# Performance work log

Measured on AMD Instinct MI355X. Metric: run time of the kernel, lower is better.

The kernel has to match this reference:

```python
import jax, jax.numpy as jnp
import numpy as np

B = 2048
LATENT = 128
C = 8                      # n_classes == class_dim
HID = 1024
D = 512                    # feature dim of minority samples
COUNTS = np.array([1024, 1536, 2048, 2560, 3072, 3584, 3840, 4096])
NMAX = int(COUNTS.max())
NEG = -1e9


def setup_inputs() -> dict:
    key = jax.random.key(0)
    ks = jax.random.split(key, 9)
    z = jax.random.normal(ks[0], (B, LATENT), dtype=jnp.float32)
    class_ids = jax.random.randint(ks[1], (B,), 0, C)
    # cTMU params (stored [in, out]; equivalent to torch Linear with W.T)
    W1 = 0.02 * jax.random.normal(ks[2], (LATENT + C, HID), dtype=jnp.float32)
    b1 = jnp.zeros((HID,), jnp.float32)
    W2 = 0.02 * jax.random.normal(ks[3], (HID, HID), dtype=jnp.float32)
    b2 = jnp.zeros((HID,), jnp.float32)
    # IGU params, padded/stacked over classes: [C, HID, NMAX], [C, NMAX]
    Wa = 0.02 * jax.random.normal(ks[4], (C, HID, NMAX), dtype=jnp.float32)
    ba = jnp.zeros((C, NMAX), jnp.float32)
    # class memory buffers, zero-padded to NMAX: [C, NMAX, D]
    Xbuf = jax.random.normal(ks[5], (C, NMAX, D), dtype=jnp.float32)
    valid = jnp.arange(NMAX)[None, :] < jnp.asarray(COUNTS)[:, None]  # [C, NMAX]
    Xbuf = Xbuf * valid[:, :, None]
    return {"z": z, "class_ids": class_ids, "W1": W1, "b1": b1,
            "W2": W2, "b2": b2, "Wa": Wa, "ba": ba, "Xbuf": Xbuf}


def reference(z, class_ids, W1, b1, W2, b2, Wa, ba, Xbuf):
    # cTMU: concat(z, onehot) -> Linear -> GELU -> Linear -> GELU
    onehot = jax.nn.one_hot(class_ids, C, dtype=z.dtype)       # [B, C]
    x = jnp.concatenate([z, onehot], axis=1)                   # [B, LATENT+C]
    h = jax.nn.gelu(x @ W1 + b1, approximate=False)            # [B, HID]
    t = jax.nn.gelu(h @ W2 + b2, approximate=False)            # [B, HID]
    # IGU logits for every class (grouped GEMM over padded buffers)
    logits = jnp.einsum('bh,chn->bcn', t, Wa) + ba[None]       # [B, C, NMAX]
    valid = jnp.arange(NMAX)[None, :] < jnp.asarray(COUNTS)[:, None]
    logits = jnp.where(valid[None], logits, NEG)
    alpha = jax.nn.softmax(logits, axis=-1)                    # [B, C, NMAX]
    # convex combination against each class buffer, then route by class id
    synth = jnp.einsum('bcn,cnd->bcd', alpha, Xbuf)            # [B, C, D]
    out = synth[jnp.arange(z.shape[0]), class_ids]             # [B, D]
    return out
```

## Files before the change

### kernel.cpp

```cpp
#include <hip/hip_runtime.h>
#include <math.h>


constexpr int B = 2048, LATENT = 128, C = 8, HID = 1024, D = 512, NMAX = 4096;

typedef __attribute__((ext_vector_type(8))) short bf16x8;
typedef __attribute__((ext_vector_type(4))) float f32x4;

#define GLD16(gsrc, ldst)                                                     \
    __builtin_amdgcn_global_load_lds(                                         \
        (const __attribute__((address_space(1))) unsigned int*)(gsrc),        \
        (__attribute__((address_space(3))) unsigned int*)(ldst), 16, 0, 0)

__device__ __forceinline__ int class_count(int c) {
    if (c < 6) return 1024 + 512 * c;
    return (c == 6) ? 3840 : 4096;
}

__device__ __forceinline__ float gelu_exact(float x) {
    return 0.5f * x * (1.0f + erff(x * 0.70710678118654752f));
}

__device__ __forceinline__ unsigned short f2bf(float f) {
    unsigned int u = __float_as_uint(f);
    return (unsigned short)((u + 0x7fffu + ((u >> 16) & 1u)) >> 16);
}

__device__ __forceinline__ float waveMax(float v) {
    #pragma unroll
    for (int o = 32; o > 0; o >>= 1) v = fmaxf(v, __shfl_down(v, o));
    return v;
}
__device__ __forceinline__ float waveSum(float v) {
    #pragma unroll
    for (int o = 32; o > 0; o >>= 1) v += __shfl_down(v, o);
    return v;
}

__global__ void k_gather(const int* __restrict__ cid, int* __restrict__ cnt,
                         int* __restrict__ idx) {
    int b = blockIdx.x * 256 + threadIdx.x;
    if (b < B) {
        int c = cid[b];
        int s = atomicAdd(&cnt[c], 1);
        idx[c * B + s] = b;
    }
}

__global__ void k_f2bf(const float* __restrict__ src,
                       unsigned short* __restrict__ dst, int n4) {
    int i = blockIdx.x * 256 + threadIdx.x;
    if (i < n4) {
        float4 v = *(const float4*)&src[(size_t)i * 4];
        ushort4 o = {f2bf(v.x), f2bf(v.y), f2bf(v.z), f2bf(v.w)};
        *(ushort4*)&dst[(size_t)i * 4] = o;
    }
}

__global__ __launch_bounds__(256) void k_repack_frag(
    const float* __restrict__ src, unsigned short* __restrict__ dst,
    int R, int Cc, size_t srcStride, size_t dstStride, int limitMode) {
    const int cls = blockIdx.z;
    const int rb = blockIdx.x;
    const int c0 = blockIdx.y * 256;
    if (limitMode == 1 && c0 >= class_count(cls)) return;
    if (limitMode == 2 && rb * 32 >= class_count(cls)) return;
    src += (size_t)cls * srcStride;
    dst += (size_t)cls * dstStride;
    __shared__ float T[32][257];
    const int t = threadIdx.x;
    #pragma unroll
    for (int i = 0; i < 8; ++i) {
        int r = i * 4 + (t >> 6);
        int cc = (t & 63) * 4;
        float4 v = *(const float4*)&src[(size_t)(rb * 32 + r) * Cc + c0 + cc];
        T[r][cc] = v.x; T[r][cc + 1] = v.y; T[r][cc + 2] = v.z; T[r][cc + 3] = v.w;
    }
    __syncthreads();
    const int RB = R >> 5;
    #pragma unroll
    for (int i = 0; i < 4; ++i) {
        int ct = i * 4 + (t >> 6);
        int lane = t & 63;
        int n = lane & 15, q = lane >> 4;
        unsigned short tmp[8];
        #pragma unroll
        for (int j = 0; j < 8; ++j) tmp[j] = f2bf(T[q * 8 + j][ct * 16 + n]);
        *(uint4*)&dst[(((size_t)(c0 / 16 + ct)) * RB + rb) * 512 + lane * 8] =
            *(const uint4*)tmp;
    }
}


#define GEMM_PIPE_STAGE(bufsel, APSTEP, BPSTEP)                               \
    do {                                                                      \
        _Pragma("unroll") for (int i = 0; i < 2; ++i)                         \
            GLD16(ap[i] + (APSTEP), AsW + (bufsel) * 4096 + i * 512);         \
        _Pragma("unroll") for (int i = 0; i < 2; ++i)                         \
            GLD16(bp[i] + (BPSTEP), BsW + (bufsel) * 4096 + i * 512);         \
    } while (0)

#define GEMM_PIPE_LOOP(KE, APSTEP, BPSTEP)                                    \
    {                                                                         \
        const int nk_ = (KE) >> 6;                                            \
        {                                                                     \
            const int k0 = 0;                                                 \
            (void)k0;                                                         \
            GEMM_PIPE_STAGE(0, APSTEP, BPSTEP);                               \
        }                                                                     \
        for (int ks_ = 0; ks_ < nk_; ++ks_) {                                 \
            const int p_ = ks_ & 1;                                           \
            if (ks_ + 1 < nk_) {                                              \
                const int k0 = (ks_ + 1) << 6;                                \
                GEMM_PIPE_STAGE(1 - p_, APSTEP, BPSTEP);                      \
                asm volatile("s_waitcnt vmcnt(4)" ::: "memory");              \
            } else {                                                          \
                asm volatile("s_waitcnt vmcnt(0)" ::: "memory");              \
            }                                                                 \
            asm volatile("s_barrier" ::: "memory");                           \
            __builtin_amdgcn_s_setprio(1);                                    \
            _Pragma("unroll") for (int kb = 0; kb < 2; ++kb) {                \
                bf16x8 bfr[4];                                                \
                _Pragma("unroll") for (int f = 0; f < 4; ++f)                 \
                    bfr[f] = *(const bf16x8*)&Bs[p_ * 4096 +                  \
                        (kb * 4 + f) * 512 + lane * 8];                       \
                bf16x8 af = *(const bf16x8*)&As[p_ * 4096 +                   \
                    (wave * 16 + ln) * 64 +                                   \
                    (((kb * 4 + lq) ^ (ln & 7)) * 8)];                        \
                _Pragma("unroll") for (int f = 0; f < 4; ++f)                 \
                    acc[f] = __builtin_amdgcn_mfma_f32_16x16x32_bf16(         \
                        af, bfr[f], acc[f], 0, 0, 0);                         \
            }                                                                 \
            __builtin_amdgcn_s_setprio(0);                                    \
            asm volatile("s_barrier" ::: "memory");                           \
        }                                                                     \
    }

__global__ __launch_bounds__(256, 8) void k_mlp_mfma(
    const unsigned short* __restrict__ A, const unsigned short* __restrict__ Bf,
    const float* __restrict__ bias, const float* __restrict__ Woh,
    const int* __restrict__ cid, unsigned short* __restrict__ Out, int K) {
    const int row0 = blockIdx.x * 64, col0 = blockIdx.y * 64;
    const int KBtot = K >> 5;
    const int t = threadIdx.x, wave = t >> 6, lane = t & 63;
    const int ln = lane & 15, lq = lane >> 4;
    __shared__ __align__(16) unsigned short As[2 * 64 * 64];
    __shared__ __align__(16) unsigned short Bs[2 * 8 * 512];
    const int arowl = lane >> 3;
    const int achk = (lane & 7) ^ arowl;
    const unsigned short* ap[2];
    #pragma unroll
    for (int i = 0; i < 2; ++i)
        ap[i] = A + (size_t)(row0 + wave * 16 + i * 8 + arowl) * K + achk * 8;
    const int kbw = wave >> 1;
    const unsigned short* bp[2];
    #pragma unroll
    for (int i = 0; i < 2; ++i) {
        int f = (wave * 2 + i) & 3;
        bp[i] = Bf + ((size_t)((col0 >> 4) + f) * KBtot + kbw) * 512 + lane * 8;
    }
    unsigned short* AsW = &As[wave * 1024];
    unsigned short* BsW = &Bs[(wave * 2) * 512];
    f32x4 acc[4] = {};
    GEMM_PIPE_LOOP(K, k0, (size_t)(k0 >> 5) * 512)
    #pragma unroll
    for (int reg = 0; reg < 4; ++reg) {
        int r = row0 + wave * 16 + lq * 4 + reg;
        const float* woh = Woh ? &Woh[(size_t)cid[r] * HID] : nullptr;
        #pragma unroll
        for (int f = 0; f < 4; ++f) {
            int col = col0 + f * 16 + ln;
            float v = acc[f][reg] + bias[col];
            if (woh) v += woh[col];
            Out[(size_t)r * HID + col] = f2bf(gelu_exact(v));
        }
    }
}

__global__ __launch_bounds__(256, 8) void k_logits_mfma(
    const unsigned short* __restrict__ T, const unsigned short* __restrict__ Wf,
    const float* __restrict__ ba, const int* __restrict__ cnt,
    const int* __restrict__ idxs, float* __restrict__ L) {
    const int c = blockIdx.y;
    const int count = class_count(c);
    const int n0 = blockIdx.x * 64;
    if (n0 >= count) return;
    const int Mc = cnt[c];
    const int row0 = blockIdx.z * 64;
    if (row0 >= Mc) return;
    const int* idxc = idxs + c * B;
    const unsigned short* Wfc = Wf + (size_t)c * 4194304;
    const int t = threadIdx.x, wave = t >> 6, lane = t & 63;
    const int ln = lane & 15, lq = lane >> 4;
    __shared__ __align__(16) unsigned short As[2 * 64 * 64];
    __shared__ __align__(16) unsigned short Bs[2 * 8 * 512];
    const int arowl = lane >> 3;
    const int achk = (lane & 7) ^ arowl;
    const unsigned short* ap[2];
    #pragma unroll
    for (int i = 0; i < 2; ++i) {
        int g = idxc[min(row0 + wave * 16 + i * 8 + arowl, Mc - 1)];
        ap[i] = T + (size_t)g * HID + achk * 8;
    }
    const int kbw = wave >> 1;
    const unsigned short* bp[2];
    #pragma unroll
    for (int i = 0; i < 2; ++i) {
        int f = (wave * 2 + i) & 3;
        bp[i] = Wfc + ((size_t)((n0 >> 4) + f) * 32 + kbw) * 512 + lane * 8;
    }
    unsigned short* AsW = &As[wave * 1024];
    unsigned short* BsW = &Bs[(wave * 2) * 512];
    f32x4 acc[4] = {};
    GEMM_PIPE_LOOP(HID, k0, (size_t)(k0 >> 5) * 512)
    #pragma unroll
    for (int reg = 0; reg < 4; ++reg) {
        int r = row0 + wave * 16 + lq * 4 + reg;
        if (r < Mc) {
            int g = idxc[r];
            #pragma unroll
            for (int f = 0; f < 4; ++f) {
                int col = n0 + f * 16 + ln;
                L[(size_t)g * NMAX + col] = acc[f][reg] + ba[c * NMAX + col];
            }
        }
    }
}

__global__ __launch_bounds__(256) void k_softmax(const float* __restrict__ L,
                                                 unsigned short* __restrict__ Aout,
                                                 const int* __restrict__ cid) {
    const int b = blockIdx.x;
    const int n = class_count(cid[b]);
    const float* row = L + (size_t)b * NMAX;
    unsigned short* orow = Aout + (size_t)b * NMAX;
    const int t = threadIdx.x;
    float v[16];
    int nv = 0;
    float mx = -INFINITY;
    for (int i = t; i < n; i += 256) {
        float x = row[i];
        v[nv++] = x;
        mx = fmaxf(mx, x);
    }
    __shared__ float red[4], red2[4];
    float wm = waveMax(mx);
    int wid = t >> 6, lid = t & 63;
    if (lid == 0) red[wid] = wm;
    __syncthreads();
    float bmax = fmaxf(fmaxf(red[0], red[1]), fmaxf(red[2], red[3]));
    float s = 0.f;
    #pragma unroll
    for (int j = 0; j < 16; ++j)
        if (j < nv) { v[j] = expf(v[j] - bmax); s += v[j]; }
    float ws_ = waveSum(s);
    if (lid == 0) red2[wid] = ws_;
    __syncthreads();
    float inv = 1.0f / (red2[0] + red2[1] + red2[2] + red2[3]);
    int j = 0;
    for (int i = t; i < n; i += 256) orow[i] = f2bf(v[j++] * inv);
}

__global__ __launch_bounds__(256, 8) void k_synth_mfma(
    const unsigned short* __restrict__ Al, const unsigned short* __restrict__ Xf,
    const int* __restrict__ cnt, const int* __restrict__ idxs,
    float* __restrict__ Out) {
    const int c = blockIdx.y;
    const int count = class_count(c);
    const int dtile = blockIdx.x & 7, kci = blockIdx.x >> 3;
    const int kc0 = kci * 1024;
    if (kc0 >= count) return;
    const int KE = min(kc0 + 1024, count) - kc0;
    const int Mc = cnt[c];
    const int row0 = blockIdx.z * 64;
    if (row0 >= Mc) return;
    const int* idxc = idxs + c * B;
    const unsigned short* Xfc = Xf + (size_t)c * 2097152;
    const int d0 = dtile * 64;
    const int t = threadIdx.x, wave = t >> 6, lane = t & 63;
    const int ln = lane & 15, lq = lane >> 4;
    __shared__ __align__(16) unsigned short As[2 * 64 * 64];
    __shared__ __align__(16) unsigned short Bs[2 * 8 * 512];
    const int arowl = lane >> 3;
    const int achk = (lane & 7) ^ arowl;
    const unsigned short* ap[2];
    #pragma unroll
    for (int i = 0; i < 2; ++i) {
        int g = idxc[min(row0 + wave * 16 + i * 8 + arowl, Mc - 1)];
        ap[i] = Al + (size_t)g * NMAX + kc0 + achk * 8;
    }
    const int kbw = wave >> 1;
    const unsigned short* bp[2];
    #pragma unroll
    for (int i = 0; i < 2; ++i) {
        int f = (wave * 2 + i) & 3;
        bp[i] = Xfc + ((size_t)((d0 >> 4) + f) * 128 + (kc0 >> 5) + kbw) * 512 + lane * 8;
    }
    unsigned short* AsW = &As[wave * 1024];
    unsigned short* BsW = &Bs[(wave * 2) * 512];
    f32x4 acc[4] = {};
    GEMM_PIPE_LOOP(KE, k0, (size_t)(k0 >> 5) * 512)
    #pragma unroll
    for (int reg = 0; reg < 4; ++reg) {
        int r = row0 + wave * 16 + lq * 4 + reg;
        if (r < Mc) {
            int g = idxc[r];
            #pragma unroll
            for (int f = 0; f < 4; ++f)
                atomicAdd(&Out[(size_t)g * D + d0 + f * 16 + ln], acc[f][reg]);
        }
    }
}

extern "C" void kernel_launch(void* const* d_in, const int* in_sizes, int n_in,
                              void* d_out, int out_size, void* d_ws,
                              size_t ws_size, hipStream_t stream) {
    const float* z    = (const float*)d_in[0];
    const int*   cid  = (const int*)d_in[1];
    const float* W1   = (const float*)d_in[2];
    const float* b1   = (const float*)d_in[3];
    const float* W2   = (const float*)d_in[4];
    const float* b2   = (const float*)d_in[5];
    const float* Wa   = (const float*)d_in[6];
    const float* ba   = (const float*)d_in[7];
    const float* Xbuf = (const float*)d_in[8];
    float* out = (float*)d_out;

    char* ws = (char*)d_ws;
    int*            cnt   = (int*)ws;
    int*            idx   = (int*)(ws + 256);
    unsigned short* zbf   = (unsigned short*)(ws + 65792);
    unsigned short* h     = (unsigned short*)(ws + 590080);
    unsigned short* tbuf  = (unsigned short*)(ws + 4784384);
    float*          L     = (float*)(ws + 8978688);
    unsigned short* abuf  = (unsigned short*)(ws + 42533120);
    unsigned short* Wf    = (unsigned short*)(ws + 59310336);
    unsigned short* Xf    = (unsigned short*)(ws + 126419200);
    unsigned short* W2f   = (unsigned short*)(ws + 159973632);
    unsigned short* W1f   = (unsigned short*)(ws + 162070784);

    hipMemsetAsync(cnt, 0, 256, stream);
    k_gather<<<dim3(B / 256), 256, 0, stream>>>(cid, cnt, idx);
    k_f2bf<<<dim3(256), 256, 0, stream>>>(z, zbf, B * LATENT / 4);
    k_repack_frag<<<dim3(4, 4, 1), 256, 0, stream>>>(W1, W1f, 128, HID, 0, 0, 0);
    k_repack_frag<<<dim3(32, 4, 1), 256, 0, stream>>>(W2, W2f, HID, HID, 0, 0, 0);
    k_repack_frag<<<dim3(32, 16, C), 256, 0, stream>>>(
        Wa, Wf, HID, NMAX, (size_t)HID * NMAX, 4194304, 1);
    k_repack_frag<<<dim3(128, 2, C), 256, 0, stream>>>(
        Xbuf, Xf, NMAX, D, (size_t)NMAX * D, 2097152, 2);
    k_mlp_mfma<<<dim3(B / 64, HID / 64), 256, 0, stream>>>(
        zbf, W1f, b1, W1 + (size_t)LATENT * HID, cid, h, LATENT);
    k_mlp_mfma<<<dim3(B / 64, HID / 64), 256, 0, stream>>>(
        h, W2f, b2, nullptr, cid, tbuf, HID);
    k_logits_mfma<<<dim3(NMAX / 64, C, B / 64), 256, 0, stream>>>(
        tbuf, Wf, ba, cnt, idx, L);
    k_softmax<<<dim3(B), 256, 0, stream>>>(L, abuf, cid);
    hipMemsetAsync(out, 0, (size_t)B * D * sizeof(float), stream);
    k_synth_mfma<<<dim3(32, C, B / 64), 256, 0, stream>>>(
        abuf, Xf, cnt, idx, out);
}
```

Baseline: 364.5 us.

## Fuse fp32-to-bf16 conversion of Wa and Xbuf into grouped GEMM B-loads

Drops the two separate repack kernels that converted Wa (128MB fp32) and Xbuf (64MB fp32) into bf16 fragment layout each call. The logits and synth GEMMs now load fp32 B values directly through registers, convert them with v_cvt_pk_bf16 and write them to shared memory during the MFMA phase of the previous stage. This removes a full read-write pass over the large weight buffers. In exchange, the GEMM B loads become strided scalar fp32 loads that each tile re-reads across row blocks, register pressure rises (launch bounds drop to 4 waves), and each tile now converts its B data again.

```diff
diff --git a/kernel.cpp b/kernel.cpp
--- a/kernel.cpp
+++ b/kernel.cpp
@@ -24,6 +24,12 @@
 __device__ __forceinline__ unsigned short f2bf(float f) {
     unsigned int u = __float_as_uint(f);
     return (unsigned short)((u + 0x7fffu + ((u >> 16) & 1u)) >> 16);
+}
+
+__device__ __forceinline__ unsigned int cvt_pk_bf16(float lo, float hi) {
+    unsigned int r;
+    asm volatile("v_cvt_pk_bf16_f32 %0, %1, %2" : "=v"(r) : "v"(lo), "v"(hi));
+    return r;
 }
 
 __device__ __forceinline__ float waveMax(float v) {
@@ -91,7 +97,6 @@
     }
 }
 
-
 #define GEMM_PIPE_STAGE(bufsel, APSTEP, BPSTEP)                               \
     do {                                                                      \
         _Pragma("unroll") for (int i = 0; i < 2; ++i)                         \
@@ -99,6 +104,20 @@
         _Pragma("unroll") for (int i = 0; i < 2; ++i)                         \
             GLD16(bp[i] + (BPSTEP), BsW + (bufsel) * 4096 + i * 512);         \
     } while (0)
+
+#define GEMM_MFMA_PHASE(p_)                                                   \
+    _Pragma("unroll") for (int kb = 0; kb < 2; ++kb) {                        \
+        bf16x8 bfr[4];                                                        \
+        _Pragma("unroll") for (int f = 0; f < 4; ++f)                         \
+            bfr[f] = *(const bf16x8*)&Bs[(p_) * 4096 +                        \
+                (kb * 4 + f) * 512 + lane * 8];                               \
+        bf16x8 af = *(const bf16x8*)&As[(p_) * 4096 +                         \
+            (wave * 16 + ln) * 64 +                                           \
+            (((kb * 4 + lq) ^ (ln & 7)) * 8)];                                \
+        _Pragma("unroll") for (int f = 0; f < 4; ++f)                         \
+            acc[f] = __builtin_amdgcn_mfma_f32_16x16x32_bf16(                 \
+                af, bfr[f], acc[f], 0, 0, 0);                                 \
+    }
 
 #define GEMM_PIPE_LOOP(KE, APSTEP, BPSTEP)                                    \
     {                                                                         \
@@ -119,19 +138,56 @@
             }                                                                 \
             asm volatile("s_barrier" ::: "memory");                           \
             __builtin_amdgcn_s_setprio(1);                                    \
-            _Pragma("unroll") for (int kb = 0; kb < 2; ++kb) {                \
-                bf16x8 bfr[4];                                                \
-                _Pragma("unroll") for (int f = 0; f < 4; ++f)                 \
-                    bfr[f] = *(const bf16x8*)&Bs[p_ * 4096 +                  \
-                        (kb * 4 + f) * 512 + lane * 8];                       \
-                bf16x8 af = *(const bf16x8*)&As[p_ * 4096 +                   \
-                    (wave * 16 + ln) * 64 +                                   \
-                    (((kb * 4 + lq) ^ (ln & 7)) * 8)];                        \
-                _Pragma("unroll") for (int f = 0; f < 4; ++f)                 \
-                    acc[f] = __builtin_amdgcn_mfma_f32_16x16x32_bf16(         \
-                        af, bfr[f], acc[f], 0, 0, 0);                         \
+            GEMM_MFMA_PHASE(p_)                                               \
+            __builtin_amdgcn_s_setprio(0);                                    \
+            asm volatile("s_barrier" ::: "memory");                           \
+        }                                                                     \
+    }
+
+#define GEMM_F32B_CVTW(bufsel)                                                \
+    _Pragma("unroll") for (int i = 0; i < 2; ++i) {                           \
+        uint4 w_;                                                             \
+        w_.x = cvt_pk_bf16(bv[i][0], bv[i][1]);                               \
+        w_.y = cvt_pk_bf16(bv[i][2], bv[i][3]);                               \
+        w_.z = cvt_pk_bf16(bv[i][4], bv[i][5]);                               \
+        w_.w = cvt_pk_bf16(bv[i][6], bv[i][7]);                               \
+        *(uint4*)&BsW[(bufsel) * 4096 + i * 512 + lane * 8] = w_;             \
+    }
+
+#define GEMM_PIPE_LOOP_F32B(KE, APSTEP_EXPR, LDB)                             \
+    {                                                                         \
+        const int nk_ = (KE) >> 6;                                            \
+        float bv[2][8];                                                       \
+        {                                                                     \
+            const int k0 = 0;                                                 \
+            (void)k0;                                                         \
+            _Pragma("unroll") for (int i = 0; i < 2; ++i)                     \
+                GLD16(ap[i] + (APSTEP_EXPR), AsW + i * 512);                  \
+            _Pragma("unroll") for (int i = 0; i < 2; ++i)                     \
+                _Pragma("unroll") for (int j = 0; j < 8; ++j)                 \
+                    bv[i][j] = bsrc[i][(size_t)j * (LDB)];                    \
+            GEMM_F32B_CVTW(0)                                                 \
+            asm volatile("s_waitcnt lgkmcnt(0)" ::: "memory");                \
+            asm volatile("s_barrier" ::: "memory");                           \
+        }                                                                     \
+        for (int ks_ = 0; ks_ < nk_; ++ks_) {                                 \
+            const int p_ = ks_ & 1;                                           \
+            if (ks_ + 1 < nk_) {                                              \
+                const int k0 = (ks_ + 1) << 6;                                \
+                _Pragma("unroll") for (int i = 0; i < 2; ++i)                 \
+                    GLD16(ap[i] + (APSTEP_EXPR),                              \
+                          AsW + (1 - p_) * 4096 + i * 512);                   \
+                _Pragma("unroll") for (int i = 0; i < 2; ++i)                 \
+                    _Pragma("unroll") for (int j = 0; j < 8; ++j)             \
+                        bv[i][j] = bsrc[i][(size_t)(k0 + j) * (LDB)];         \
             }                                                                 \
+            __builtin_amdgcn_s_setprio(1);                                    \
+            GEMM_MFMA_PHASE(p_)                                               \
             __builtin_amdgcn_s_setprio(0);                                    \
+            if (ks_ + 1 < nk_) {                                              \
+                GEMM_F32B_CVTW(1 - p_)                                        \
+            }                                                                 \
+            asm volatile("s_waitcnt lgkmcnt(0)" ::: "memory");                \
             asm volatile("s_barrier" ::: "memory");                           \
         }                                                                     \
     }
@@ -177,8 +233,8 @@
     }
 }
 
-__global__ __launch_bounds__(256, 8) void k_logits_mfma(
-    const unsigned short* __restrict__ T, const unsigned short* __restrict__ Wf,
+__global__ __launch_bounds__(256, 4) void k_logits_mfma(
+    const unsigned short* __restrict__ T, const float* __restrict__ Wa,
     const float* __restrict__ ba, const int* __restrict__ cnt,
     const int* __restrict__ idxs, float* __restrict__ L) {
     const int c = blockIdx.y;
@@ -189,7 +245,7 @@
     const int row0 = blockIdx.z * 64;
     if (row0 >= Mc) return;
     const int* idxc = idxs + c * B;
-    const unsigned short* Wfc = Wf + (size_t)c * 4194304;
+    const float* Wc = Wa + (size_t)c * HID * NMAX;
     const int t = threadIdx.x, wave = t >> 6, lane = t & 63;
     const int ln = lane & 15, lq = lane >> 4;
     __shared__ __align__(16) unsigned short As[2 * 64 * 64];
@@ -202,17 +258,17 @@
         int g = idxc[min(row0 + wave * 16 + i * 8 + arowl, Mc - 1)];
         ap[i] = T + (size_t)g * HID + achk * 8;
     }
-    const int kbw = wave >> 1;
-    const unsigned short* bp[2];
+    const float* bsrc[2];
     #pragma unroll
     for (int i = 0; i < 2; ++i) {
         int f = (wave * 2 + i) & 3;
-        bp[i] = Wfc + ((size_t)((n0 >> 4) + f) * 32 + kbw) * 512 + lane * 8;
+        bsrc[i] = Wc + (size_t)((wave >> 1) * 32 + lq * 8) * NMAX +
+                  n0 + f * 16 + ln;
     }
     unsigned short* AsW = &As[wave * 1024];
     unsigned short* BsW = &Bs[(wave * 2) * 512];
     f32x4 acc[4] = {};
-    GEMM_PIPE_LOOP(HID, k0, (size_t)(k0 >> 5) * 512)
+    GEMM_PIPE_LOOP_F32B(HID, k0, NMAX)
     #pragma unroll
     for (int reg = 0; reg < 4; ++reg) {
         int r = row0 + wave * 16 + lq * 4 + reg;
@@ -261,8 +317,8 @@
     for (int i = t; i < n; i += 256) orow[i] = f2bf(v[j++] * inv);
 }
 
-__global__ __launch_bounds__(256, 8) void k_synth_mfma(
-    const unsigned short* __restrict__ Al, const unsigned short* __restrict__ Xf,
+__global__ __launch_bounds__(256, 4) void k_synth_mfma(
+    const unsigned short* __restrict__ Al, const float* __restrict__ Xbuf,
     const int* __restrict__ cnt, const int* __restrict__ idxs,
     float* __restrict__ Out) {
     const int c = blockIdx.y;
@@ -275,7 +331,7 @@
     const int row0 = blockIdx.z * 64;
     if (row0 >= Mc) return;
     const int* idxc = idxs + c * B;
-    const unsigned short* Xfc = Xf + (size_t)c * 2097152;
+    const float* Xc = Xbuf + (size_t)c * NMAX * D;
     const int d0 = dtile * 64;
     const int t = threadIdx.x, wave = t >> 6, lane = t & 63;
     const int ln = lane & 15, lq = lane >> 4;
@@ -289,17 +345,17 @@
         int g = idxc[min(row0 + wave * 16 + i * 8 + arowl, Mc - 1)];
         ap[i] = Al + (size_t)g * NMAX + kc0 + achk * 8;
     }
-    const int kbw = wave >> 1;
-    const unsigned short* bp[2];
+    const float* bsrc[2];
     #pragma unroll
     for (int i = 0; i < 2; ++i) {
         int f = (wave * 2 + i) & 3;
-        bp[i] = Xfc + ((size_t)((d0 >> 4) + f) * 128 + (kc0 >> 5) + kbw) * 512 + lane * 8;
+        bsrc[i] = Xc + (size_t)(kc0 + (wave >> 1) * 32 + lq * 8) * D +
+                  d0 + f * 16 + ln;
     }
     unsigned short* AsW = &As[wave * 1024];
     unsigned short* BsW = &Bs[(wave * 2) * 512];
     f32x4 acc[4] = {};
-    GEMM_PIPE_LOOP(KE, k0, (size_t)(k0 >> 5) * 512)
+    GEMM_PIPE_LOOP_F32B(KE, k0, D)
     #pragma unroll
     for (int reg = 0; reg < 4; ++reg) {
         int r = row0 + wave * 16 + lq * 4 + reg;
@@ -334,8 +390,6 @@
     unsigned short* tbuf  = (unsigned short*)(ws + 4784384);
     float*          L     = (float*)(ws + 8978688);
     unsigned short* abuf  = (unsigned short*)(ws + 42533120);
-    unsigned short* Wf    = (unsigned short*)(ws + 59310336);
-    unsigned short* Xf    = (unsigned short*)(ws + 126419200);
     unsigned short* W2f   = (unsigned short*)(ws + 159973632);
     unsigned short* W1f   = (unsigned short*)(ws + 162070784);
 
@@ -344,18 +398,14 @@
     k_f2bf<<<dim3(256), 256, 0, stream>>>(z, zbf, B * LATENT / 4);
     k_repack_frag<<<dim3(4, 4, 1), 256, 0, stream>>>(W1, W1f, 128, HID, 0, 0, 0);
     k_repack_frag<<<dim3(32, 4, 1), 256, 0, stream>>>(W2, W2f, HID, HID, 0, 0, 0);
-    k_repack_frag<<<dim3(32, 16, C), 256, 0, stream>>>(
-        Wa, Wf, HID, NMAX, (size_t)HID * NMAX, 4194304, 1);
-    k_repack_frag<<<dim3(128, 2, C), 256, 0, stream>>>(
-        Xbuf, Xf, NMAX, D, (size_t)NMAX * D, 2097152, 2);
     k_mlp_mfma<<<dim3(B / 64, HID / 64), 256, 0, stream>>>(
         zbf, W1f, b1, W1 + (size_t)LATENT * HID, cid, h, LATENT);
     k_mlp_mfma<<<dim3(B / 64, HID / 64), 256, 0, stream>>>(
         h, W2f, b2, nullptr, cid, tbuf, HID);
     k_logits_mfma<<<dim3(NMAX / 64, C, B / 64), 256, 0, stream>>>(
-        tbuf, Wf, ba, cnt, idx, L);
+        tbuf, Wa, ba, cnt, idx, L);
     k_softmax<<<dim3(B), 256, 0, stream>>>(L, abuf, cid);
     hipMemsetAsync(out, 0, (size_t)B * D * sizeof(float), stream);
     k_synth_mfma<<<dim3(32, C, B / 64), 256, 0, stream>>>(
-        abuf, Xf, cnt, idx, out);
-}
+        abuf, Xbuf, cnt, idx, out);
+}
```

After: 373.3 us. 2.4% more time.

## Retile logits and synth GEMMs to 256-row blocks with resident B panels

Applied to the files above, without the earlier changes.

The logits and synth kernels now use 512-thread blocks covering 256 gathered rows, with each wave computing two 16-row M tiles. The B operand (the Wa or Xbuf fragments) is loaded once into a large LDS panel and reused across all rows, while only the A rows are double-buffered. This cuts repeated weight traffic and per-block overhead, and synth uses a finer 512-wide K split. The cost is far more LDS per block (about 96KB), one block per CU, fewer blocks in flight, and more atomics from the finer K split.

```diff
diff --git a/kernel.cpp b/kernel.cpp
--- a/kernel.cpp
+++ b/kernel.cpp
@@ -91,7 +91,6 @@
     }
 }
 
-
 #define GEMM_PIPE_STAGE(bufsel, APSTEP, BPSTEP)                               \
     do {                                                                      \
         _Pragma("unroll") for (int i = 0; i < 2; ++i)                         \
@@ -99,6 +98,20 @@
         _Pragma("unroll") for (int i = 0; i < 2; ++i)                         \
             GLD16(bp[i] + (BPSTEP), BsW + (bufsel) * 4096 + i * 512);         \
     } while (0)
+
+#define GEMM_MFMA_PHASE(p_)                                                   \
+    _Pragma("unroll") for (int kb = 0; kb < 2; ++kb) {                        \
+        bf16x8 bfr[4];                                                        \
+        _Pragma("unroll") for (int f = 0; f < 4; ++f)                         \
+            bfr[f] = *(const bf16x8*)&Bs[(p_) * 4096 +                        \
+                (kb * 4 + f) * 512 + lane * 8];                               \
+        bf16x8 af = *(const bf16x8*)&As[(p_) * 4096 +                         \
+            (wave * 16 + ln) * 64 +                                           \
+            (((kb * 4 + lq) ^ (ln & 7)) * 8)];                                \
+        _Pragma("unroll") for (int f = 0; f < 4; ++f)                         \
+            acc[f] = __builtin_amdgcn_mfma_f32_16x16x32_bf16(                 \
+                af, bfr[f], acc[f], 0, 0, 0);                                 \
+    }
 
 #define GEMM_PIPE_LOOP(KE, APSTEP, BPSTEP)                                    \
     {                                                                         \
@@ -119,18 +132,48 @@
             }                                                                 \
             asm volatile("s_barrier" ::: "memory");                           \
             __builtin_amdgcn_s_setprio(1);                                    \
-            _Pragma("unroll") for (int kb = 0; kb < 2; ++kb) {                \
-                bf16x8 bfr[4];                                                \
-                _Pragma("unroll") for (int f = 0; f < 4; ++f)                 \
-                    bfr[f] = *(const bf16x8*)&Bs[p_ * 4096 +                  \
-                        (kb * 4 + f) * 512 + lane * 8];                       \
-                bf16x8 af = *(const bf16x8*)&As[p_ * 4096 +                   \
-                    (wave * 16 + ln) * 64 +                                   \
-                    (((kb * 4 + lq) ^ (ln & 7)) * 8)];                        \
-                _Pragma("unroll") for (int f = 0; f < 4; ++f)                 \
-                    acc[f] = __builtin_amdgcn_mfma_f32_16x16x32_bf16(         \
-                        af, bfr[f], acc[f], 0, 0, 0);                         \
+            GEMM_MFMA_PHASE(p_)                                               \
+            __builtin_amdgcn_s_setprio(0);                                    \
+            asm volatile("s_barrier" ::: "memory");                           \
+        }                                                                     \
+    }
+
+#define ASTAGE_PR(bufsel, koff)                                               \
+    _Pragma("unroll") for (int i = 0; i < 4; ++i)                             \
+        GLD16(ap[i] + (koff), AsW + (bufsel) * 16384 + i * 512);
+
+#define PANEL_MFMA(p_, ks_)                                                   \
+    _Pragma("unroll") for (int kb = 0; kb < 2; ++kb) {                        \
+        bf16x8 bfr[4];                                                        \
+        _Pragma("unroll") for (int f = 0; f < 4; ++f)                         \
+            bfr[f] = *(const bf16x8*)&Bp[                                     \
+                (f * 16 + (ks_) * 2 + kb) * 512 + lane * 8];                  \
+        _Pragma("unroll") for (int mt = 0; mt < 2; ++mt) {                    \
+            bf16x8 af = *(const bf16x8*)&As[(p_) * 16384 +                    \
+                (wave * 32 + mt * 16 + ln) * 64 +                             \
+                (((kb * 4 + lq) ^ (ln & 7)) * 8)];                            \
+            _Pragma("unroll") for (int f = 0; f < 4; ++f)                     \
+                acc[mt][f] = __builtin_amdgcn_mfma_f32_16x16x32_bf16(         \
+                    af, bfr[f], acc[mt][f], 0, 0, 0);                         \
+        }                                                                     \
+    }
+
+#define PANEL_KLOOP(NK, KBASE)                                                \
+    {                                                                         \
+        ASTAGE_PR(0, (KBASE));                                                \
+        asm volatile("s_waitcnt vmcnt(0)" ::: "memory");                      \
+        asm volatile("s_barrier" ::: "memory");                               \
+        for (int ks = 0; ks < (NK); ++ks) {                                   \
+            const int p_ = ks & 1;                                            \
+            if (ks + 1 < (NK)) {                                              \
+                ASTAGE_PR(1 - p_, (KBASE) + (ks + 1) * 64);                   \
+                asm volatile("s_waitcnt vmcnt(4)" ::: "memory");              \
+            } else {                                                          \
+                asm volatile("s_waitcnt vmcnt(0)" ::: "memory");              \
             }                                                                 \
+            asm volatile("s_barrier" ::: "memory");                           \
+            __builtin_amdgcn_s_setprio(1);                                    \
+            PANEL_MFMA(p_, ks)                                                \
             __builtin_amdgcn_s_setprio(0);                                    \
             asm volatile("s_barrier" ::: "memory");                           \
         }                                                                     \
@@ -177,7 +220,7 @@
     }
 }
 
-__global__ __launch_bounds__(256, 8) void k_logits_mfma(
+__global__ __launch_bounds__(512, 1) void k_logits_mfma(
     const unsigned short* __restrict__ T, const unsigned short* __restrict__ Wf,
     const float* __restrict__ ba, const int* __restrict__ cnt,
     const int* __restrict__ idxs, float* __restrict__ L) {
@@ -186,42 +229,47 @@
     const int n0 = blockIdx.x * 64;
     if (n0 >= count) return;
     const int Mc = cnt[c];
-    const int row0 = blockIdx.z * 64;
+    const int row0 = blockIdx.z * 256;
     if (row0 >= Mc) return;
     const int* idxc = idxs + c * B;
     const unsigned short* Wfc = Wf + (size_t)c * 4194304;
     const int t = threadIdx.x, wave = t >> 6, lane = t & 63;
     const int ln = lane & 15, lq = lane >> 4;
-    __shared__ __align__(16) unsigned short As[2 * 64 * 64];
-    __shared__ __align__(16) unsigned short Bs[2 * 8 * 512];
+    __shared__ __align__(16) unsigned short As[2 * 256 * 64];
+    __shared__ __align__(16) unsigned short Bp[64 * 512];
     const int arowl = lane >> 3;
     const int achk = (lane & 7) ^ arowl;
-    const unsigned short* ap[2];
-    #pragma unroll
-    for (int i = 0; i < 2; ++i) {
-        int g = idxc[min(row0 + wave * 16 + i * 8 + arowl, Mc - 1)];
+    const unsigned short* ap[4];
+    #pragma unroll
+    for (int i = 0; i < 4; ++i) {
+        int g = idxc[min(row0 + wave * 32 + i * 8 + arowl, Mc - 1)];
         ap[i] = T + (size_t)g * HID + achk * 8;
     }
-    const int kbw = wave >> 1;
-    const unsigned short* bp[2];
-    #pragma unroll
-    for (int i = 0; i < 2; ++i) {
-        int f = (wave * 2 + i) & 3;
-        bp[i] = Wfc + ((size_t)((n0 >> 4) + f) * 32 + kbw) * 512 + lane * 8;
-    }
-    unsigned short* AsW = &As[wave * 1024];
-    unsigned short* BsW = &Bs[(wave * 2) * 512];
-    f32x4 acc[4] = {};
-    GEMM_PIPE_LOOP(HID, k0, (size_t)(k0 >> 5) * 512)
-    #pragma unroll
-    for (int reg = 0; reg < 4; ++reg) {
-        int r = row0 + wave * 16 + lq * 4 + reg;
-        if (r < Mc) {
-            int g = idxc[r];
-            #pragma unroll
-            for (int f = 0; f < 4; ++f) {
-                int col = n0 + f * 16 + ln;
-                L[(size_t)g * NMAX + col] = acc[f][reg] + ba[c * NMAX + col];
+    unsigned short* AsW = &As[wave * 2048];
+    f32x4 acc[2][4] = {};
+    #pragma unroll
+    for (int q = 0; q < 2; ++q) {
+        #pragma unroll
+        for (int j = 0; j < 8; ++j) {
+            int fi = wave * 8 + j;
+            GLD16(Wfc + ((size_t)((n0 >> 4) + (fi >> 4)) * 32 + q * 16 +
+                         (fi & 15)) * 512 + lane * 8,
+                  Bp + fi * 512);
+        }
+        PANEL_KLOOP(8, q * 512)
+    }
+    #pragma unroll
+    for (int mt = 0; mt < 2; ++mt) {
+        #pragma unroll
+        for (int reg = 0; reg < 4; ++reg) {
+            int r = row0 + wave * 32 + mt * 16 + lq * 4 + reg;
+            if (r < Mc) {
+                int g = idxc[r];
+                #pragma unroll
+                for (int f = 0; f < 4; ++f) {
+                    int col = n0 + f * 16 + ln;
+                    L[(size_t)g * NMAX + col] = acc[mt][f][reg] + ba[c * NMAX + col];
+                }
             }
         }
     }
@@ -261,53 +309,60 @@
     for (int i = t; i < n; i += 256) orow[i] = f2bf(v[j++] * inv);
 }
 
-__global__ __launch_bounds__(256, 8) void k_synth_mfma(
+__global__ __launch_bounds__(512, 1) void k_synth_mfma(
     const unsigned short* __restrict__ Al, const unsigned short* __restrict__ Xf,
     const int* __restrict__ cnt, const int* __restrict__ idxs,
     float* __restrict__ Out) {
     const int c = blockIdx.y;
     const int count = class_count(c);
     const int dtile = blockIdx.x & 7, kci = blockIdx.x >> 3;
-    const int kc0 = kci * 1024;
+    const int kc0 = kci * 512;
     if (kc0 >= count) return;
-    const int KE = min(kc0 + 1024, count) - kc0;
+    const int KE = min(kc0 + 512, count) - kc0;
     const int Mc = cnt[c];
-    const int row0 = blockIdx.z * 64;
+    const int row0 = blockIdx.z * 256;
     if (row0 >= Mc) return;
     const int* idxc = idxs + c * B;
     const unsigned short* Xfc = Xf + (size_t)c * 2097152;
     const int d0 = dtile * 64;
     const int t = threadIdx.x, wave = t >> 6, lane = t & 63;
     const int ln = lane & 15, lq = lane >> 4;
-    __shared__ __align__(16) unsigned short As[2 * 64 * 64];
-    __shared__ __align__(16) unsigned short Bs[2 * 8 * 512];
+    __shared__ __align__(16) unsigned short As[2 * 256 * 64];
+    __shared__ __align__(16) unsigned short Bp[64 * 512];
     const int arowl = lane >> 3;
     const int achk = (lane & 7) ^ arowl;
-    const unsigned short* ap[2];
-    #pragma unroll
-    for (int i = 0; i < 2; ++i) {
-        int g = idxc[min(row0 + wave * 16 + i * 8 + arowl, Mc - 1)];
+    const unsigned short* ap[4];
+    #pragma unroll
+    for (int i = 0; i < 4; ++i) {
+        int g = idxc[min(row0 + wave * 32 + i * 8 + arowl, Mc - 1)];
         ap[i] = Al + (size_t)g * NMAX + kc0 + achk * 8;
     }
-    const int kbw = wave >> 1;
-    const unsigned short* bp[2];
-    #pragma unroll
-    for (int i = 0; i < 2; ++i) {
-        int f = (wave * 2 + i) & 3;
-        bp[i] = Xfc + ((size_t)((d0 >> 4) + f) * 128 + (kc0 >> 5) + kbw) * 512 + lane * 8;
-    }
-    unsigned short* AsW = &As[wave * 1024];
-    unsigned short* BsW = &Bs[(wave * 2) * 512];
-    f32x4 acc[4] = {};
-    GEMM_PIPE_LOOP(KE, k0, (size_t)(k0 >> 5) * 512)
-    #pragma unroll
-    for (int reg = 0; reg < 4; ++reg) {
-        int r = row0 + wave * 16 + lq * 4 + reg;
-        if (r < Mc) {
-            int g = idxc[r];
-            #pragma unroll
-            for (int f = 0; f < 4; ++f)
-                atomicAdd(&Out[(size_t)g * D + d0 + f * 16 + ln], acc[f][reg]);
+    unsigned short* AsW = &As[wave * 2048];
+    f32x4 acc[2][4] = {};
+    const int nk = KE >> 6;
+    const int nkbl = KE >> 5;
+    const int kshift = (nkbl == 16) ? 4 : 3;
+    const int pw = nkbl >> 1;
+    for (int j = 0; j < pw; ++j) {
+        int fi = wave * pw + j;
+        int f = fi >> kshift, kbl = fi & (nkbl - 1);
+        GLD16(Xfc + ((size_t)((d0 >> 4) + f) * 128 + (kc0 >> 5) + kbl) * 512 +
+                  lane * 8,
+              Bp + (f * 16 + kbl) * 512);
+    }
+    PANEL_KLOOP(nk, 0)
+    #pragma unroll
+    for (int mt = 0; mt < 2; ++mt) {
+        #pragma unroll
+        for (int reg = 0; reg < 4; ++reg) {
+            int r = row0 + wave * 32 + mt * 16 + lq * 4 + reg;
+            if (r < Mc) {
+                int g = idxc[r];
+                #pragma unroll
+                for (int f = 0; f < 4; ++f)
+                    atomicAdd(&Out[(size_t)g * D + d0 + f * 16 + ln],
+                              acc[mt][f][reg]);
+            }
         }
     }
 }
@@ -352,10 +407,10 @@
         zbf, W1f, b1, W1 + (size_t)LATENT * HID, cid, h, LATENT);
     k_mlp_mfma<<<dim3(B / 64, HID / 64), 256, 0, stream>>>(
         h, W2f, b2, nullptr, cid, tbuf, HID);
-    k_logits_mfma<<<dim3(NMAX / 64, C, B / 64), 256, 0, stream>>>(
+    k_logits_mfma<<<dim3(NMAX / 64, C, B / 256), 512, 0, stream>>>(
         tbuf, Wf, ba, cnt, idx, L);
     k_softmax<<<dim3(B), 256, 0, stream>>>(L, abuf, cid);
     hipMemsetAsync(out, 0, (size_t)B * D * sizeof(float), stream);
-    k_synth_mfma<<<dim3(32, C, B / 64), 256, 0, stream>>>(
+    k_synth_mfma<<<dim3(64, C, B / 256), 512, 0, stream>>>(
         abuf, Xf, cnt, idx, out);
 }
```

New measurement: 398.6 us. 9.3% more time.
